# Performance work log

Measured on AMD Instinct MI355X. Metric: run time of the kernel, lower is better.

The kernel has to match this reference:

```python
import jax, jax.numpy as jnp
import numpy as np

B, D_IN, H = 32768, 256, 128
N_TASK, N_EXP, N_SHARE = 2, 4, 4


def setup_inputs() -> dict:
    key = jax.random.key(0)
    ks = jax.random.split(key, 4)
    s = 1.0 / np.sqrt(D_IN)
    return {
        "x": jax.random.normal(ks[0], (B, D_IN), dtype=jnp.float32),
        "W_share": jax.random.normal(ks[1], (N_SHARE, D_IN, H), dtype=jnp.float32) * s,
        "b_share": jnp.zeros((N_SHARE, H), dtype=jnp.float32),
        "W_task": jax.random.normal(ks[2], (N_TASK, N_EXP, D_IN, H), dtype=jnp.float32) * s,
        "b_task": jnp.zeros((N_TASK, N_EXP, H), dtype=jnp.float32),
        "W_gate": jax.random.normal(ks[3], (N_TASK, D_IN, N_SHARE + N_EXP), dtype=jnp.float32) * s,
        "b_gate": jnp.zeros((N_TASK, N_SHARE + N_EXP), dtype=jnp.float32),
    }


def reference(x, W_share, b_share, W_task, b_task, W_gate, b_gate):
    # shared experts: [B, N_SHARE, H]
    share = jax.nn.relu(jnp.einsum('bd,edh->beh', x, W_share) + b_share)
    # task-specific experts: [T, B, N_EXP, H]
    task = jax.nn.relu(jnp.einsum('bd,tedh->tbeh', x, W_task) + b_task[:, None])
    # gates: [T, B, N_SHARE + N_EXP], softmax over experts
    gate = jax.nn.softmax(jnp.einsum('bd,tdg->tbg', x, W_gate) + b_gate[:, None], axis=-1)
    # concat order matches original: share_net first, then task experts
    share_b = jnp.broadcast_to(share[None], (N_TASK, B, N_SHARE, H))
    experts = jnp.concatenate([share_b, task], axis=2)  # [T, B, N_SHARE+N_EXP, H]
    towers = jnp.einsum('tbeh,tbe->tbh', experts, gate)  # [T, B, H]
    return towers
```

## Files before the change

### kernel.cpp

```cpp
#include <hip/hip_runtime.h>


typedef __attribute__((ext_vector_type(8))) short short8;
typedef __attribute__((ext_vector_type(4))) float float4v;

#define ROW_US     136
#define ROW_B      272
#define UNIT_US    17408
#define UNIT_B     34816
#define WAVE_B     4352
#define WGT_OFF_US 417792
#define COPY_US    421888
#define COPY_B     843776

__device__ __forceinline__ unsigned short f2bf(float f) {
  unsigned u = __builtin_bit_cast(unsigned, f);
  u += 0x7FFFu + ((u >> 16) & 1u);
  return (unsigned short)(u >> 16);
}

__global__ __launch_bounds__(256)
void prep_kernel(const float* __restrict__ Ws,
                 const float* __restrict__ Wt,
                 const float* __restrict__ Wg,
                 unsigned short* __restrict__ WT, int NC) {
  int bid = blockIdx.x;
  int tid = threadIdx.x;
  if (bid < 96) {
    __shared__ float tile[64][65];
    int e  = bid >> 3;
    int kt = (bid >> 1) & 3;
    int ht = bid & 1;
    const float* src = (e < 4) ? Ws + ((size_t)e << 15)
                               : Wt + ((size_t)(e - 4) << 15);
    int m = tid & 15, n = tid >> 4;
    #pragma unroll
    for (int i = 0; i < 4; ++i) {
      int kl = i * 16 + n;
      float4 v = *(const float4*)&src[(size_t)(kt * 64 + kl) * 128 + ht * 64 + m * 4];
      tile[kl][m * 4 + 0] = v.x;
      tile[kl][m * 4 + 1] = v.y;
      tile[kl][m * 4 + 2] = v.z;
      tile[kl][m * 4 + 3] = v.w;
    }
    __syncthreads();
    #pragma unroll
    for (int i = 0; i < 4; ++i) {
      int hl = i * 16 + n;
      ushort4 o;
      o.x = f2bf(tile[m * 4 + 0][hl]);
      o.y = f2bf(tile[m * 4 + 1][hl]);
      o.z = f2bf(tile[m * 4 + 2][hl]);
      o.w = f2bf(tile[m * 4 + 3][hl]);
      size_t rowbase = (size_t)(e * 2 + (kt >> 1)) * UNIT_US
                     + (size_t)(ht * 64 + hl) * ROW_US + (kt & 1) * 64;
      for (int c = 0; c < NC; ++c) {
        *(ushort4*)&WT[(size_t)c * COPY_US + rowbase + m * 4] = o;
        if ((kt & 1) == 1 && m < 2) {
          ushort4 z = {0, 0, 0, 0};
          *(ushort4*)&WT[(size_t)c * COPY_US + rowbase + 64 + m * 4] = z;
        }
      }
    }
  } else {
    #pragma unroll
    for (int it = 0; it < 16; ++it) {
      int j = it * 256 + tid;
      int n = j >> 8, k = j & 255;
      int t = n >> 3, g = n & 7;
      unsigned short v = f2bf(Wg[(size_t)(t * 256 + k) * 8 + g]);
      for (int c = 0; c < NC; ++c)
        WT[(size_t)c * COPY_US + WGT_OFF_US + j] = v;
    }
  }
}

__global__ __launch_bounds__(512, 2)
void dmoe_main(const float* __restrict__ x,
               const unsigned short* __restrict__ WT,
               const float* __restrict__ b_share,
               const float* __restrict__ b_task,
               const float* __restrict__ b_gate,
               float* __restrict__ out, int NC) {
  __shared__ unsigned short Bs0[UNIT_US];
  __shared__ unsigned short Bs1[UNIT_US];
  __shared__ float gatesL[16 * 132];
  __shared__ float biasLds[12 * 128];

  const int tid  = threadIdx.x;
  const int lane = tid & 63;
  const int w    = tid >> 6;
  const int col  = lane & 15;
  const int quad = lane >> 4;
  const int mg   = w >> 1;
  const int ng   = w & 1;
  const int blk  = blockIdx.x;

  const char* WTc = (const char*)WT + (size_t)((blk >> 3) % NC) * COPY_B;

  uint4 p0, p1, p2, p3; unsigned p4;
  {
    const char* g = WTc + w * WAVE_B;
    p0 = *(const uint4*)(g + lane * 16);
    p1 = *(const uint4*)(g + 1024 + lane * 16);
    p2 = *(const uint4*)(g + 2048 + lane * 16);
    p3 = *(const uint4*)(g + 3072 + lane * 16);
    p4 = *(const unsigned*)(g + 4096 + lane * 4);
  }

  short8 A[2][8];
  {
    const float* xb = x + ((size_t)blk * 128 + mg * 32 + col) * 256 + quad * 8;
    #pragma unroll
    for (int mt = 0; mt < 2; ++mt) {
      const float* xr = xb + (size_t)mt * 16 * 256;
      #pragma unroll
      for (int k = 0; k < 8; ++k) {
        float4 u = *(const float4*)(xr + k * 32);
        float4 v = *(const float4*)(xr + k * 32 + 4);
        short8 fr;
        fr[0] = (short)f2bf(u.x); fr[1] = (short)f2bf(u.y);
        fr[2] = (short)f2bf(u.z); fr[3] = (short)f2bf(u.w);
        fr[4] = (short)f2bf(v.x); fr[5] = (short)f2bf(v.y);
        fr[6] = (short)f2bf(v.z); fr[7] = (short)f2bf(v.w);
        A[mt][k] = fr;
      }
    }
  }

  for (int i = tid; i < 1536; i += 512)
    biasLds[i] = (i < 512) ? b_share[i] : b_task[i - 512];

  {
    const unsigned short* WgT = (const unsigned short*)(WTc + WGT_OFF_US * 2);
    const unsigned short* bp = WgT + (size_t)col * 256 + quad * 8;
    short8 Bg[8];
    #pragma unroll
    for (int k = 0; k < 8; ++k) Bg[k] = *(const short8*)(bp + k * 32);
    float bg = b_gate[col];
    #pragma unroll
    for (int mt = 0; mt < 2; ++mt) {
      float4v ag = {0.f, 0.f, 0.f, 0.f};
      #pragma unroll
      for (int k = 0; k < 8; ++k)
        ag = __builtin_amdgcn_mfma_f32_16x16x32_bf16(A[mt][k], Bg[k], ag, 0, 0, 0);
      #pragma unroll
      for (int r = 0; r < 4; ++r) {
        float vlog = ag[r] + bg;
        float m = vlog;
        m = fmaxf(m, __shfl_xor(m, 1));
        m = fmaxf(m, __shfl_xor(m, 2));
        m = fmaxf(m, __shfl_xor(m, 4));
        float p = __expf(vlog - m);
        float s = p;
        s += __shfl_xor(s, 1);
        s += __shfl_xor(s, 2);
        s += __shfl_xor(s, 4);
        if (ng == 0)
          gatesL[col * 132 + mg * 32 + mt * 16 + quad * 4 + r] = p / s;
      }
    }
  }

  {
    char* l = (char*)Bs0 + w * WAVE_B;
    *(uint4*)(l + lane * 16)        = p0;
    *(uint4*)(l + 1024 + lane * 16) = p1;
    *(uint4*)(l + 2048 + lane * 16) = p2;
    *(uint4*)(l + 3072 + lane * 16) = p3;
    *(unsigned*)(l + 4096 + lane * 4) = p4;
  }
  __syncthreads();

  float tw[2][2][4][4];
  #pragma unroll
  for (int t = 0; t < 2; ++t)
    #pragma unroll
    for (int mt = 0; mt < 2; ++mt)
      #pragma unroll
      for (int nt = 0; nt < 4; ++nt)
        #pragma unroll
        for (int r = 0; r < 4; ++r)
          tw[t][mt][nt][r] = 0.f;

  const int hb = ng * 64;
  float4v acc[2][4];

  #pragma unroll 1
  for (int e = 0; e < 12; ++e) {
    #pragma unroll
    for (int kh = 0; kh < 2; ++kh) {
      const int u = e * 2 + kh;
      uint4 q0, q1, q2, q3; unsigned q4;
      const bool doStage = (u < 23);
      if (doStage) {
        const char* g = WTc + (size_t)(u + 1) * UNIT_B + w * WAVE_B;
        q0 = *(const uint4*)(g + lane * 16);
        q1 = *(const uint4*)(g + 1024 + lane * 16);
        q2 = *(const uint4*)(g + 2048 + lane * 16);
        q3 = *(const uint4*)(g + 3072 + lane * 16);
        q4 = *(const unsigned*)(g + 4096 + lane * 4);
      }
      if (kh == 0) {
        #pragma unroll
        for (int mt = 0; mt < 2; ++mt)
          #pragma unroll
          for (int nt = 0; nt < 4; ++nt)
            acc[mt][nt] = (float4v){0.f, 0.f, 0.f, 0.f};
      }
      {
        const char* Bb = (const char*)(kh ? Bs1 : Bs0);
        #pragma unroll
        for (int kk = 0; kk < 4; ++kk) {
          #pragma unroll
          for (int nt = 0; nt < 4; ++nt) {
            short8 bfr = *(const short8*)(Bb + (hb + nt * 16 + col) * ROW_B
                                          + kk * 64 + quad * 16);
            acc[0][nt] = __builtin_amdgcn_mfma_f32_16x16x32_bf16(
                A[0][kh * 4 + kk], bfr, acc[0][nt], 0, 0, 0);
            acc[1][nt] = __builtin_amdgcn_mfma_f32_16x16x32_bf16(
                A[1][kh * 4 + kk], bfr, acc[1][nt], 0, 0, 0);
          }
        }
      }
      if (doStage) {
        char* l = (char*)(kh ? Bs0 : Bs1) + w * WAVE_B;
        *(uint4*)(l + lane * 16)        = q0;
        *(uint4*)(l + 1024 + lane * 16) = q1;
        *(uint4*)(l + 2048 + lane * 16) = q2;
        *(uint4*)(l + 3072 + lane * 16) = q3;
        *(unsigned*)(l + 4096 + lane * 4) = q4;
      }
      if (kh == 1) {
        float bias[4];
        #pragma unroll
        for (int nt = 0; nt < 4; ++nt)
          bias[nt] = biasLds[e * 128 + hb + nt * 16 + col];
        if (e < 4) {
          #pragma unroll
          for (int mt = 0; mt < 2; ++mt) {
            int rb = mg * 32 + mt * 16 + quad * 4;
            float4 g0 = *(const float4*)&gatesL[e * 132 + rb];
            float4 g1 = *(const float4*)&gatesL[(8 + e) * 132 + rb];
            #pragma unroll
            for (int nt = 0; nt < 4; ++nt)
              #pragma unroll
              for (int r = 0; r < 4; ++r) {
                float v = fmaxf(acc[mt][nt][r] + bias[nt], 0.f);
                tw[0][mt][nt][r] += ((const float*)&g0)[r] * v;
                tw[1][mt][nt][r] += ((const float*)&g1)[r] * v;
              }
          }
        } else {
          const int t  = (e - 4) >> 2;
          const int gc = t * 8 + 4 + ((e - 4) & 3);
          #pragma unroll
          for (int mt = 0; mt < 2; ++mt) {
            int rb = mg * 32 + mt * 16 + quad * 4;
            float4 g = *(const float4*)&gatesL[gc * 132 + rb];
            #pragma unroll
            for (int nt = 0; nt < 4; ++nt)
              #pragma unroll
              for (int r = 0; r < 4; ++r) {
                float v = fmaxf(acc[mt][nt][r] + bias[nt], 0.f);
                tw[t][mt][nt][r] += ((const float*)&g)[r] * v;
              }
          }
        }
      }
      __syncthreads();
    }
  }

  #pragma unroll
  for (int t = 0; t < 2; ++t)
    #pragma unroll
    for (int mt = 0; mt < 2; ++mt)
      #pragma unroll
      for (int r = 0; r < 4; ++r) {
        size_t row = (size_t)blk * 128 + mg * 32 + mt * 16 + quad * 4 + r;
        float* op = out + ((size_t)t << 22) + row * 128 + hb;
        #pragma unroll
        for (int nt = 0; nt < 4; ++nt)
          op[nt * 16 + col] = tw[t][mt][nt][r];
      }
}

extern "C" void kernel_launch(void* const* d_in, const int* in_sizes, int n_in,
                              void* d_out, int out_size, void* d_ws, size_t ws_size,
                              hipStream_t stream) {
  const float* x       = (const float*)d_in[0];
  const float* W_share = (const float*)d_in[1];
  const float* b_share = (const float*)d_in[2];
  const float* W_task  = (const float*)d_in[3];
  const float* b_task  = (const float*)d_in[4];
  const float* W_gate  = (const float*)d_in[5];
  const float* b_gate  = (const float*)d_in[6];
  float* out = (float*)d_out;
  unsigned short* WT = (unsigned short*)d_ws;

  int NC = (int)(ws_size / (size_t)COPY_B);
  if (NC < 1) NC = 1;
  if (NC > 4) NC = 4;

  prep_kernel<<<97, 256, 0, stream>>>(W_share, W_task, W_gate, WT, NC);
  dmoe_main<<<256, 512, 0, stream>>>(x, WT, b_share, b_task, b_gate, out, NC);
}
```

Measured before the change: 191.7 us.

## Split blocks per task, recompute shared experts, rotate expert order

Each block now handles a single task for a 128-row tile, doubling the grid to 512 blocks and processing 8 expert slots (4 shared + 4 task) instead of 12. Expert processing order is rotated per block group to spread weight reads, and x loads and output stores use nontemporal hints; the weight copy count is capped at 2. This trades redundant shared-expert GEMMs, gate computation and x conversion for higher occupancy and fewer accumulator registers.

```diff
diff --git a/kernel.cpp b/kernel.cpp
--- a/kernel.cpp
+++ b/kernel.cpp
@@ -17,6 +17,10 @@
   unsigned u = __builtin_bit_cast(unsigned, f);
   u += 0x7FFFu + ((u >> 16) & 1u);
   return (unsigned short)(u >> 16);
+}
+
+__device__ __forceinline__ int slot2e(int sr, int t) {
+  return (sr < 4) ? sr : 4 + t * 4 + (sr - 4);
 }
 
 __global__ __launch_bounds__(256)
@@ -84,8 +88,8 @@
                float* __restrict__ out, int NC) {
   __shared__ unsigned short Bs0[UNIT_US];
   __shared__ unsigned short Bs1[UNIT_US];
-  __shared__ float gatesL[16 * 132];
-  __shared__ float biasLds[12 * 128];
+  __shared__ float gatesL[8 * 132];
+  __shared__ float biasLds[8 * 128];
 
   const int tid  = threadIdx.x;
   const int lane = tid & 63;
@@ -95,12 +99,16 @@
   const int mg   = w >> 1;
   const int ng   = w & 1;
   const int blk  = blockIdx.x;
+  const int t    = blk & 1;
+  const int rt   = blk >> 1;
+  const int rot  = (blk >> 3) & 7;
 
   const char* WTc = (const char*)WT + (size_t)((blk >> 3) % NC) * COPY_B;
 
+  const int e0 = slot2e(rot, t);
   uint4 p0, p1, p2, p3; unsigned p4;
   {
-    const char* g = WTc + w * WAVE_B;
+    const char* g = WTc + (size_t)(e0 * 2) * UNIT_B + w * WAVE_B;
     p0 = *(const uint4*)(g + lane * 16);
     p1 = *(const uint4*)(g + 1024 + lane * 16);
     p2 = *(const uint4*)(g + 2048 + lane * 16);
@@ -110,34 +118,38 @@
 
   short8 A[2][8];
   {
-    const float* xb = x + ((size_t)blk * 128 + mg * 32 + col) * 256 + quad * 8;
+    const float* xb = x + ((size_t)rt * 128 + mg * 32 + col) * 256 + quad * 8;
     #pragma unroll
     for (int mt = 0; mt < 2; ++mt) {
       const float* xr = xb + (size_t)mt * 16 * 256;
       #pragma unroll
       for (int k = 0; k < 8; ++k) {
-        float4 u = *(const float4*)(xr + k * 32);
-        float4 v = *(const float4*)(xr + k * 32 + 4);
+        float4v u = __builtin_nontemporal_load((const float4v*)(xr + k * 32));
+        float4v v = __builtin_nontemporal_load((const float4v*)(xr + k * 32 + 4));
         short8 fr;
-        fr[0] = (short)f2bf(u.x); fr[1] = (short)f2bf(u.y);
-        fr[2] = (short)f2bf(u.z); fr[3] = (short)f2bf(u.w);
-        fr[4] = (short)f2bf(v.x); fr[5] = (short)f2bf(v.y);
-        fr[6] = (short)f2bf(v.z); fr[7] = (short)f2bf(v.w);
+        fr[0] = (short)f2bf(u[0]); fr[1] = (short)f2bf(u[1]);
+        fr[2] = (short)f2bf(u[2]); fr[3] = (short)f2bf(u[3]);
+        fr[4] = (short)f2bf(v[0]); fr[5] = (short)f2bf(v[1]);
+        fr[6] = (short)f2bf(v[2]); fr[7] = (short)f2bf(v[3]);
         A[mt][k] = fr;
       }
     }
   }
 
-  for (int i = tid; i < 1536; i += 512)
-    biasLds[i] = (i < 512) ? b_share[i] : b_task[i - 512];
+  for (int i = tid; i < 1024; i += 512) {
+    int sr = i >> 7, h = i & 127;
+    biasLds[i] = (sr < 4) ? b_share[sr * 128 + h]
+                          : b_task[(size_t)(t * 4 + (sr - 4)) * 128 + h];
+  }
 
   {
     const unsigned short* WgT = (const unsigned short*)(WTc + WGT_OFF_US * 2);
-    const unsigned short* bp = WgT + (size_t)col * 256 + quad * 8;
+    const int gr = col & 7;
+    const unsigned short* bp = WgT + (size_t)(t * 8 + gr) * 256 + quad * 8;
     short8 Bg[8];
     #pragma unroll
     for (int k = 0; k < 8; ++k) Bg[k] = *(const short8*)(bp + k * 32);
-    float bg = b_gate[col];
+    float bg = b_gate[t * 8 + gr];
     #pragma unroll
     for (int mt = 0; mt < 2; ++mt) {
       float4v ag = {0.f, 0.f, 0.f, 0.f};
@@ -156,7 +168,7 @@
         s += __shfl_xor(s, 1);
         s += __shfl_xor(s, 2);
         s += __shfl_xor(s, 4);
-        if (ng == 0)
+        if (ng == 0 && col < 8)
           gatesL[col * 132 + mg * 32 + mt * 16 + quad * 4 + r] = p / s;
       }
     }
@@ -172,29 +184,31 @@
   }
   __syncthreads();
 
-  float tw[2][2][4][4];
+  float tw[2][4][4];
   #pragma unroll
-  for (int t = 0; t < 2; ++t)
-    #pragma unroll
-    for (int mt = 0; mt < 2; ++mt)
-      #pragma unroll
-      for (int nt = 0; nt < 4; ++nt)
-        #pragma unroll
-        for (int r = 0; r < 4; ++r)
-          tw[t][mt][nt][r] = 0.f;
+  for (int mt = 0; mt < 2; ++mt)
+    #pragma unroll
+    for (int nt = 0; nt < 4; ++nt)
+      #pragma unroll
+      for (int r = 0; r < 4; ++r)
+        tw[mt][nt][r] = 0.f;
 
   const int hb = ng * 64;
   float4v acc[2][4];
 
   #pragma unroll 1
-  for (int e = 0; e < 12; ++e) {
+  for (int s = 0; s < 8; ++s) {
+    const int sr  = (s + rot) & 7;
+    const int e   = slot2e(sr, t);
+    const int sr2 = (s + 1 + rot) & 7;
+    const int e2  = slot2e(sr2, t);
     #pragma unroll
     for (int kh = 0; kh < 2; ++kh) {
-      const int u = e * 2 + kh;
       uint4 q0, q1, q2, q3; unsigned q4;
-      const bool doStage = (u < 23);
+      const bool doStage = !(s == 7 && kh == 1);
       if (doStage) {
-        const char* g = WTc + (size_t)(u + 1) * UNIT_B + w * WAVE_B;
+        const int un = (kh == 0) ? (e * 2 + 1) : (e2 * 2);
+        const char* g = WTc + (size_t)un * UNIT_B + w * WAVE_B;
         q0 = *(const uint4*)(g + lane * 16);
         q1 = *(const uint4*)(g + 1024 + lane * 16);
         q2 = *(const uint4*)(g + 2048 + lane * 16);
@@ -232,39 +246,18 @@
         *(unsigned*)(l + 4096 + lane * 4) = q4;
       }
       if (kh == 1) {
-        float bias[4];
         #pragma unroll
-        for (int nt = 0; nt < 4; ++nt)
-          bias[nt] = biasLds[e * 128 + hb + nt * 16 + col];
-        if (e < 4) {
+        for (int mt = 0; mt < 2; ++mt) {
+          int rb = mg * 32 + mt * 16 + quad * 4;
+          float4 g = *(const float4*)&gatesL[sr * 132 + rb];
           #pragma unroll
-          for (int mt = 0; mt < 2; ++mt) {
-            int rb = mg * 32 + mt * 16 + quad * 4;
-            float4 g0 = *(const float4*)&gatesL[e * 132 + rb];
-            float4 g1 = *(const float4*)&gatesL[(8 + e) * 132 + rb];
+          for (int nt = 0; nt < 4; ++nt) {
+            float bias = biasLds[sr * 128 + hb + nt * 16 + col];
             #pragma unroll
-            for (int nt = 0; nt < 4; ++nt)
-              #pragma unroll
-              for (int r = 0; r < 4; ++r) {
-                float v = fmaxf(acc[mt][nt][r] + bias[nt], 0.f);
-                tw[0][mt][nt][r] += ((const float*)&g0)[r] * v;
-                tw[1][mt][nt][r] += ((const float*)&g1)[r] * v;
-              }
-          }
-        } else {
-          const int t  = (e - 4) >> 2;
-          const int gc = t * 8 + 4 + ((e - 4) & 3);
-          #pragma unroll
-          for (int mt = 0; mt < 2; ++mt) {
-            int rb = mg * 32 + mt * 16 + quad * 4;
-            float4 g = *(const float4*)&gatesL[gc * 132 + rb];
-            #pragma unroll
-            for (int nt = 0; nt < 4; ++nt)
-              #pragma unroll
-              for (int r = 0; r < 4; ++r) {
-                float v = fmaxf(acc[mt][nt][r] + bias[nt], 0.f);
-                tw[t][mt][nt][r] += ((const float*)&g)[r] * v;
-              }
+            for (int r = 0; r < 4; ++r) {
+              float v = fmaxf(acc[mt][nt][r] + bias, 0.f);
+              tw[mt][nt][r] += ((const float*)&g)[r] * v;
+            }
           }
         }
       }
@@ -273,17 +266,15 @@
   }
 
   #pragma unroll
-  for (int t = 0; t < 2; ++t)
-    #pragma unroll
-    for (int mt = 0; mt < 2; ++mt)
-      #pragma unroll
-      for (int r = 0; r < 4; ++r) {
-        size_t row = (size_t)blk * 128 + mg * 32 + mt * 16 + quad * 4 + r;
-        float* op = out + ((size_t)t << 22) + row * 128 + hb;
-        #pragma unroll
-        for (int nt = 0; nt < 4; ++nt)
-          op[nt * 16 + col] = tw[t][mt][nt][r];
-      }
+  for (int mt = 0; mt < 2; ++mt)
+    #pragma unroll
+    for (int r = 0; r < 4; ++r) {
+      size_t row = (size_t)rt * 128 + mg * 32 + mt * 16 + quad * 4 + r;
+      float* op = out + ((size_t)t << 22) + row * 128 + hb;
+      #pragma unroll
+      for (int nt = 0; nt < 4; ++nt)
+        __builtin_nontemporal_store(tw[mt][nt][r], op + nt * 16 + col);
+    }
 }
 
 extern "C" void kernel_launch(void* const* d_in, const int* in_sizes, int n_in,
@@ -301,8 +292,8 @@
 
   int NC = (int)(ws_size / (size_t)COPY_B);
   if (NC < 1) NC = 1;
-  if (NC > 4) NC = 4;
+  if (NC > 2) NC = 2;
 
   prep_kernel<<<97, 256, 0, stream>>>(W_share, W_task, W_gate, WT, NC);
-  dmoe_main<<<256, 512, 0, stream>>>(x, WT, b_share, b_task, b_gate, out, NC);
-}
+  dmoe_main<<<512, 512, 0, stream>>>(x, WT, b_share, b_task, b_gate, out, NC);
+}
```

Result: faster. 156.5 us (-18.4%).

## Swizzle weight LDS layout, retile waves to 64x32, add nontemporal x/out access

Applied to the files above, without the earlier changes.

Replaces the padded weight rows (136 shorts) with unpadded 128-short rows using an XOR chunk swizzle, which avoids LDS bank conflicts without padding and shrinks staging to exactly 4 uint4 loads per lane. Wave tiling changes from 2 M-groups x 2 N-groups (32x64 per wave) to 2x4 (64x32 per wave), so each B fragment is reused across four M tiles. This doubles the A-fragment registers held per wave. x loads and output stores become nontemporal, and the number of weight copies is capped at 2 instead of 4.

```diff
diff --git a/kernel.cpp b/kernel.cpp
--- a/kernel.cpp
+++ b/kernel.cpp
@@ -4,14 +4,11 @@
 typedef __attribute__((ext_vector_type(8))) short short8;
 typedef __attribute__((ext_vector_type(4))) float float4v;
 
-#define ROW_US     136
-#define ROW_B      272
-#define UNIT_US    17408
-#define UNIT_B     34816
-#define WAVE_B     4352
-#define WGT_OFF_US 417792
-#define COPY_US    421888
-#define COPY_B     843776
+#define UNIT_B     32768
+#define WAVE_B     4096
+#define WGT_OFF_US 393216
+#define COPY_US    397312
+#define COPY_B     794624
 
 __device__ __forceinline__ unsigned short f2bf(float f) {
   unsigned u = __builtin_bit_cast(unsigned, f);
@@ -44,23 +41,22 @@
       tile[kl][m * 4 + 3] = v.w;
     }
     __syncthreads();
+    int klocal = m * 4;
+    int chunk  = (kt & 1) * 2 + (klocal >> 5);
+    int kin    = klocal & 31;
     #pragma unroll
     for (int i = 0; i < 4; ++i) {
       int hl = i * 16 + n;
+      int h  = ht * 64 + hl;
       ushort4 o;
-      o.x = f2bf(tile[m * 4 + 0][hl]);
-      o.y = f2bf(tile[m * 4 + 1][hl]);
-      o.z = f2bf(tile[m * 4 + 2][hl]);
-      o.w = f2bf(tile[m * 4 + 3][hl]);
-      size_t rowbase = (size_t)(e * 2 + (kt >> 1)) * UNIT_US
-                     + (size_t)(ht * 64 + hl) * ROW_US + (kt & 1) * 64;
-      for (int c = 0; c < NC; ++c) {
-        *(ushort4*)&WT[(size_t)c * COPY_US + rowbase + m * 4] = o;
-        if ((kt & 1) == 1 && m < 2) {
-          ushort4 z = {0, 0, 0, 0};
-          *(ushort4*)&WT[(size_t)c * COPY_US + rowbase + 64 + m * 4] = z;
-        }
-      }
+      o.x = f2bf(tile[klocal + 0][hl]);
+      o.y = f2bf(tile[klocal + 1][hl]);
+      o.z = f2bf(tile[klocal + 2][hl]);
+      o.w = f2bf(tile[klocal + 3][hl]);
+      size_t us = (size_t)(e * 2 + (kt >> 1)) * 16384
+                + (size_t)h * 128 + (size_t)((chunk ^ (h & 3)) * 32 + kin);
+      for (int c = 0; c < NC; ++c)
+        *(ushort4*)&WT[(size_t)c * COPY_US + us] = o;
     }
   } else {
     #pragma unroll
@@ -82,8 +78,8 @@
                const float* __restrict__ b_task,
                const float* __restrict__ b_gate,
                float* __restrict__ out, int NC) {
-  __shared__ unsigned short Bs0[UNIT_US];
-  __shared__ unsigned short Bs1[UNIT_US];
+  __shared__ unsigned short Bs0[UNIT_B / 2];
+  __shared__ unsigned short Bs1[UNIT_B / 2];
   __shared__ float gatesL[16 * 132];
   __shared__ float biasLds[12 * 128];
 
@@ -92,38 +88,37 @@
   const int w    = tid >> 6;
   const int col  = lane & 15;
   const int quad = lane >> 4;
-  const int mg   = w >> 1;
-  const int ng   = w & 1;
+  const int mg   = w >> 2;
+  const int ng   = w & 3;
   const int blk  = blockIdx.x;
 
   const char* WTc = (const char*)WT + (size_t)((blk >> 3) % NC) * COPY_B;
 
-  uint4 p0, p1, p2, p3; unsigned p4;
+  uint4 p0, p1, p2, p3;
   {
-    const char* g = WTc + w * WAVE_B;
-    p0 = *(const uint4*)(g + lane * 16);
-    p1 = *(const uint4*)(g + 1024 + lane * 16);
-    p2 = *(const uint4*)(g + 2048 + lane * 16);
-    p3 = *(const uint4*)(g + 3072 + lane * 16);
-    p4 = *(const unsigned*)(g + 4096 + lane * 4);
-  }
-
-  short8 A[2][8];
+    const char* g = WTc + w * WAVE_B + lane * 16;
+    p0 = *(const uint4*)(g);
+    p1 = *(const uint4*)(g + 1024);
+    p2 = *(const uint4*)(g + 2048);
+    p3 = *(const uint4*)(g + 3072);
+  }
+
+  short8 A[4][8];
   {
-    const float* xb = x + ((size_t)blk * 128 + mg * 32 + col) * 256 + quad * 8;
-    #pragma unroll
-    for (int mt = 0; mt < 2; ++mt) {
+    const float* xb = x + ((size_t)blk * 128 + mg * 64 + col) * 256 + quad * 8;
+    #pragma unroll
+    for (int mt = 0; mt < 4; ++mt) {
       const float* xr = xb + (size_t)mt * 16 * 256;
       #pragma unroll
-      for (int k = 0; k < 8; ++k) {
-        float4 u = *(const float4*)(xr + k * 32);
-        float4 v = *(const float4*)(xr + k * 32 + 4);
+      for (int kc = 0; kc < 8; ++kc) {
+        float4v u = __builtin_nontemporal_load((const float4v*)(xr + kc * 32));
+        float4v v = __builtin_nontemporal_load((const float4v*)(xr + kc * 32 + 4));
         short8 fr;
-        fr[0] = (short)f2bf(u.x); fr[1] = (short)f2bf(u.y);
-        fr[2] = (short)f2bf(u.z); fr[3] = (short)f2bf(u.w);
-        fr[4] = (short)f2bf(v.x); fr[5] = (short)f2bf(v.y);
-        fr[6] = (short)f2bf(v.z); fr[7] = (short)f2bf(v.w);
-        A[mt][k] = fr;
+        fr[0] = (short)f2bf(u[0]); fr[1] = (short)f2bf(u[1]);
+        fr[2] = (short)f2bf(u[2]); fr[3] = (short)f2bf(u[3]);
+        fr[4] = (short)f2bf(v[0]); fr[5] = (short)f2bf(v[1]);
+        fr[6] = (short)f2bf(v[2]); fr[7] = (short)f2bf(v[3]);
+        A[mt][kc] = fr;
       }
     }
   }
@@ -136,14 +131,14 @@
     const unsigned short* bp = WgT + (size_t)col * 256 + quad * 8;
     short8 Bg[8];
     #pragma unroll
-    for (int k = 0; k < 8; ++k) Bg[k] = *(const short8*)(bp + k * 32);
+    for (int kc = 0; kc < 8; ++kc) Bg[kc] = *(const short8*)(bp + kc * 32);
     float bg = b_gate[col];
     #pragma unroll
-    for (int mt = 0; mt < 2; ++mt) {
+    for (int mt = 0; mt < 4; ++mt) {
       float4v ag = {0.f, 0.f, 0.f, 0.f};
       #pragma unroll
-      for (int k = 0; k < 8; ++k)
-        ag = __builtin_amdgcn_mfma_f32_16x16x32_bf16(A[mt][k], Bg[k], ag, 0, 0, 0);
+      for (int kc = 0; kc < 8; ++kc)
+        ag = __builtin_amdgcn_mfma_f32_16x16x32_bf16(A[mt][kc], Bg[kc], ag, 0, 0, 0);
       #pragma unroll
       for (int r = 0; r < 4; ++r) {
         float vlog = ag[r] + bg;
@@ -157,93 +152,94 @@
         s += __shfl_xor(s, 2);
         s += __shfl_xor(s, 4);
         if (ng == 0)
-          gatesL[col * 132 + mg * 32 + mt * 16 + quad * 4 + r] = p / s;
+          gatesL[col * 132 + mg * 64 + mt * 16 + quad * 4 + r] = p / s;
       }
     }
   }
 
   {
-    char* l = (char*)Bs0 + w * WAVE_B;
-    *(uint4*)(l + lane * 16)        = p0;
-    *(uint4*)(l + 1024 + lane * 16) = p1;
-    *(uint4*)(l + 2048 + lane * 16) = p2;
-    *(uint4*)(l + 3072 + lane * 16) = p3;
-    *(unsigned*)(l + 4096 + lane * 4) = p4;
+    char* l = (char*)Bs0 + w * WAVE_B + lane * 16;
+    *(uint4*)(l)        = p0;
+    *(uint4*)(l + 1024) = p1;
+    *(uint4*)(l + 2048) = p2;
+    *(uint4*)(l + 3072) = p3;
   }
   __syncthreads();
 
-  float tw[2][2][4][4];
+  float tw[2][4][2][4];
   #pragma unroll
   for (int t = 0; t < 2; ++t)
     #pragma unroll
-    for (int mt = 0; mt < 2; ++mt)
-      #pragma unroll
-      for (int nt = 0; nt < 4; ++nt)
+    for (int mt = 0; mt < 4; ++mt)
+      #pragma unroll
+      for (int nt = 0; nt < 2; ++nt)
         #pragma unroll
         for (int r = 0; r < 4; ++r)
           tw[t][mt][nt][r] = 0.f;
 
-  const int hb = ng * 64;
-  float4v acc[2][4];
+  float4v acc[4][2];
 
   #pragma unroll 1
   for (int e = 0; e < 12; ++e) {
     #pragma unroll
     for (int kh = 0; kh < 2; ++kh) {
       const int u = e * 2 + kh;
-      uint4 q0, q1, q2, q3; unsigned q4;
+      uint4 q0, q1, q2, q3;
       const bool doStage = (u < 23);
       if (doStage) {
-        const char* g = WTc + (size_t)(u + 1) * UNIT_B + w * WAVE_B;
-        q0 = *(const uint4*)(g + lane * 16);
-        q1 = *(const uint4*)(g + 1024 + lane * 16);
-        q2 = *(const uint4*)(g + 2048 + lane * 16);
-        q3 = *(const uint4*)(g + 3072 + lane * 16);
-        q4 = *(const unsigned*)(g + 4096 + lane * 4);
+        const char* g = WTc + (size_t)(u + 1) * UNIT_B + w * WAVE_B + lane * 16;
+        q0 = *(const uint4*)(g);
+        q1 = *(const uint4*)(g + 1024);
+        q2 = *(const uint4*)(g + 2048);
+        q3 = *(const uint4*)(g + 3072);
       }
       if (kh == 0) {
         #pragma unroll
-        for (int mt = 0; mt < 2; ++mt)
+        for (int mt = 0; mt < 4; ++mt)
           #pragma unroll
-          for (int nt = 0; nt < 4; ++nt)
+          for (int nt = 0; nt < 2; ++nt)
             acc[mt][nt] = (float4v){0.f, 0.f, 0.f, 0.f};
       }
       {
         const char* Bb = (const char*)(kh ? Bs1 : Bs0);
         #pragma unroll
-        for (int kk = 0; kk < 4; ++kk) {
+        for (int kc = 0; kc < 4; ++kc) {
           #pragma unroll
-          for (int nt = 0; nt < 4; ++nt) {
-            short8 bfr = *(const short8*)(Bb + (hb + nt * 16 + col) * ROW_B
-                                          + kk * 64 + quad * 16);
+          for (int nt = 0; nt < 2; ++nt) {
+            const int h = ng * 32 + nt * 16 + col;
+            short8 bfr = *(const short8*)(Bb + h * 256
+                                          + (kc ^ (h & 3)) * 64 + quad * 16);
             acc[0][nt] = __builtin_amdgcn_mfma_f32_16x16x32_bf16(
-                A[0][kh * 4 + kk], bfr, acc[0][nt], 0, 0, 0);
+                A[0][kh * 4 + kc], bfr, acc[0][nt], 0, 0, 0);
             acc[1][nt] = __builtin_amdgcn_mfma_f32_16x16x32_bf16(
-                A[1][kh * 4 + kk], bfr, acc[1][nt], 0, 0, 0);
+                A[1][kh * 4 + kc], bfr, acc[1][nt], 0, 0, 0);
+            acc[2][nt] = __builtin_amdgcn_mfma_f32_16x16x32_bf16(
+                A[2][kh * 4 + kc], bfr, acc[2][nt], 0, 0, 0);
+            acc[3][nt] = __builtin_amdgcn_mfma_f32_16x16x32_bf16(
+                A[3][kh * 4 + kc], bfr, acc[3][nt], 0, 0, 0);
           }
         }
       }
       if (doStage) {
-        char* l = (char*)(kh ? Bs0 : Bs1) + w * WAVE_B;
-        *(uint4*)(l + lane * 16)        = q0;
-        *(uint4*)(l + 1024 + lane * 16) = q1;
-        *(uint4*)(l + 2048 + lane * 16) = q2;
-        *(uint4*)(l + 3072 + lane * 16) = q3;
-        *(unsigned*)(l + 4096 + lane * 4) = q4;
+        char* l = (char*)(kh ? Bs0 : Bs1) + w * WAVE_B + lane * 16;
+        *(uint4*)(l)        = q0;
+        *(uint4*)(l + 1024) = q1;
+        *(uint4*)(l + 2048) = q2;
+        *(uint4*)(l + 3072) = q3;
       }
       if (kh == 1) {
-        float bias[4];
+        float bias[2];
         #pragma unroll
-        for (int nt = 0; nt < 4; ++nt)
-          bias[nt] = biasLds[e * 128 + hb + nt * 16 + col];
+        for (int nt = 0; nt < 2; ++nt)
+          bias[nt] = biasLds[e * 128 + ng * 32 + nt * 16 + col];
         if (e < 4) {
           #pragma unroll
-          for (int mt = 0; mt < 2; ++mt) {
-            int rb = mg * 32 + mt * 16 + quad * 4;
+          for (int mt = 0; mt < 4; ++mt) {
+            int rb = mg * 64 + mt * 16 + quad * 4;
             float4 g0 = *(const float4*)&gatesL[e * 132 + rb];
             float4 g1 = *(const float4*)&gatesL[(8 + e) * 132 + rb];
             #pragma unroll
-            for (int nt = 0; nt < 4; ++nt)
+            for (int nt = 0; nt < 2; ++nt)
               #pragma unroll
               for (int r = 0; r < 4; ++r) {
                 float v = fmaxf(acc[mt][nt][r] + bias[nt], 0.f);
@@ -255,11 +251,11 @@
           const int t  = (e - 4) >> 2;
           const int gc = t * 8 + 4 + ((e - 4) & 3);
           #pragma unroll
-          for (int mt = 0; mt < 2; ++mt) {
-            int rb = mg * 32 + mt * 16 + quad * 4;
+          for (int mt = 0; mt < 4; ++mt) {
+            int rb = mg * 64 + mt * 16 + quad * 4;
             float4 g = *(const float4*)&gatesL[gc * 132 + rb];
             #pragma unroll
-            for (int nt = 0; nt < 4; ++nt)
+            for (int nt = 0; nt < 2; ++nt)
               #pragma unroll
               for (int r = 0; r < 4; ++r) {
                 float v = fmaxf(acc[mt][nt][r] + bias[nt], 0.f);
@@ -275,14 +271,13 @@
   #pragma unroll
   for (int t = 0; t < 2; ++t)
     #pragma unroll
-    for (int mt = 0; mt < 2; ++mt)
+    for (int mt = 0; mt < 4; ++mt)
       #pragma unroll
       for (int r = 0; r < 4; ++r) {
-        size_t row = (size_t)blk * 128 + mg * 32 + mt * 16 + quad * 4 + r;
-        float* op = out + ((size_t)t << 22) + row * 128 + hb;
-        #pragma unroll
-        for (int nt = 0; nt < 4; ++nt)
-          op[nt * 16 + col] = tw[t][mt][nt][r];
+        size_t row = (size_t)blk * 128 + mg * 64 + mt * 16 + quad * 4 + r;
+        float* op = out + ((size_t)t << 22) + row * 128 + ng * 32;
+        __builtin_nontemporal_store(tw[t][mt][0][r], op + col);
+        __builtin_nontemporal_store(tw[t][mt][1][r], op + 16 + col);
       }
 }
 
@@ -301,7 +296,7 @@
 
   int NC = (int)(ws_size / (size_t)COPY_B);
   if (NC < 1) NC = 1;
-  if (NC > 4) NC = 4;
+  if (NC > 2) NC = 2;
 
   prep_kernel<<<97, 256, 0, stream>>>(W_share, W_task, W_gate, WT, NC);
   dmoe_main<<<256, 512, 0, stream>>>(x, WT, b_share, b_task, b_gate, out, NC);
```

New measurement: 233.4 us. 1.22x slower.
